# Optimization experiments

Hardware: AMD Instinct MI355X
Metric: run time of the kernel (lower is better)

Reference implementation:

```python
import jax, jax.numpy as jnp
import numpy as np

HIDDEN = 1024
NUM_HEAD = 16
HEAD_DIM = HIDDEN // NUM_HEAD


def setup_inputs() -> dict:
    key = jax.random.key(0)
    ks = jax.random.split(key, 9)
    B, S = 1, 4096
    scale = 1.0 / np.sqrt(HIDDEN)
    inp = {
        "x": jax.random.normal(ks[0], (B, S, HIDDEN), dtype=jnp.float32),
        "wq": jax.random.normal(ks[1], (HIDDEN, HIDDEN), dtype=jnp.float32) * scale,
        "bq": jnp.zeros((HIDDEN,), dtype=jnp.float32),
        "wk": jax.random.normal(ks[2], (HIDDEN, HIDDEN), dtype=jnp.float32) * scale,
        "bk": jnp.zeros((HIDDEN,), dtype=jnp.float32),
        "wv": jax.random.normal(ks[3], (HIDDEN, HIDDEN), dtype=jnp.float32) * scale,
        "bv": jnp.zeros((HIDDEN,), dtype=jnp.float32),
        "wo": jax.random.normal(ks[4], (HIDDEN, HIDDEN), dtype=jnp.float32) * scale,
        "bo": jnp.zeros((HIDDEN,), dtype=jnp.float32),
    }
    return inp


def reference(x, wq, bq, wk, bk, wv, bv, wo, bo):
    B, S, _ = x.shape
    # QKV projections (torch Linear: x @ W.T + b)
    def split_heads(t):
        return t.reshape(B, S, NUM_HEAD, HEAD_DIM).transpose(0, 2, 1, 3)  # [B,H,S,D]
    q = split_heads(x @ wq.T + bq)
    k = split_heads(x @ wk.T + bk)
    v = split_heads(x @ wv.T + bv)
    # scaled dot-product scores: [B,H,S,S]
    scores = jnp.einsum('bhsd,bhtd->bhst', q, k) / jnp.sqrt(jnp.float32(HEAD_DIM))
    # faithful double softmax over the key axis (no mask; dropout = eval identity)
    attn = jax.nn.softmax(scores, axis=-1)
    attn = jax.nn.softmax(attn, axis=-1)
    out = jnp.einsum('bhst,bhtd->bhsd', attn, v)  # [B,H,S,D]
    out = out.transpose(0, 2, 1, 3).reshape(B, S, HIDDEN)
    return out @ wo.T + bo
```

## Files before the change

### kernel.cpp

```cpp
#include <hip/hip_runtime.h>
#include <hip/hip_bf16.h>
#include <stdint.h>

#define S 4096
#define HID 1024
#define NH 16
#define DH 64

typedef __attribute__((ext_vector_type(8))) short short8;
typedef __attribute__((ext_vector_type(4))) float f32x4;
typedef __attribute__((ext_vector_type(16))) float f32x16;
typedef __attribute__((ext_vector_type(4))) unsigned int u32x4;

__device__ __forceinline__ unsigned short f2bf(float f) {
  unsigned int u = __builtin_bit_cast(unsigned int, f);
  u += 0x7FFF + ((u >> 16) & 1);
  return (unsigned short)(u >> 16);
}
__device__ __forceinline__ unsigned int pktrunc(float lo, float hi) {
  return __builtin_amdgcn_perm(__builtin_bit_cast(unsigned int, hi),
                               __builtin_bit_cast(unsigned int, lo), 0x07060302u);
}
__device__ __forceinline__ void gload16(const unsigned short* g, unsigned short* l) {
  __builtin_amdgcn_global_load_lds((const __attribute__((address_space(1))) unsigned int*)g,
                                   (__attribute__((address_space(3))) unsigned int*)l, 16, 0, 0);
}

__global__ __launch_bounds__(256) void cast_kernel(
    const float* __restrict__ x,  const float* __restrict__ wq,
    const float* __restrict__ wk, const float* __restrict__ wv,
    const float* __restrict__ wo,
    unsigned short* __restrict__ xb,  unsigned short* __restrict__ wqb,
    unsigned short* __restrict__ wkb, unsigned short* __restrict__ wvb,
    unsigned short* __restrict__ wob)
{
  int y = blockIdx.y;
  const float* src; unsigned short* dst; int n;
  if      (y == 0) { src = x;  dst = xb;  n = S * HID; }
  else if (y == 1) { src = wq; dst = wqb; n = HID * HID; }
  else if (y == 2) { src = wk; dst = wkb; n = HID * HID; }
  else if (y == 3) { src = wv; dst = wvb; n = HID * HID; }
  else             { src = wo; dst = wob; n = HID * HID; }
  int i = (blockIdx.x * 256 + threadIdx.x) * 4;
  if (i < n) {
    float4 v = *reinterpret_cast<const float4*>(src + i);
    ushort4 o;
    o.x = f2bf(v.x); o.y = f2bf(v.y); o.z = f2bf(v.z); o.w = f2bf(v.w);
    *reinterpret_cast<ushort4*>(dst + i) = o;
  }
}

__device__ __forceinline__ void gemm128(
    const unsigned short* __restrict__ A, const unsigned short* __restrict__ W,
    unsigned short* As, unsigned short* Bs, f32x4 acc[4][4], int row0, int col0)
{
  const int tid = threadIdx.x;
  const int wave = tid >> 6, lane = tid & 63, quad = lane >> 4, l16 = lane & 15;
  const int wr = (wave >> 1) * 64, wc = (wave & 1) * 64;
  const int srow = lane >> 2, sseg = lane & 3;
  const f32x4 z = {0.f, 0.f, 0.f, 0.f};
  #pragma unroll
  for (int i = 0; i < 4; i++)
    #pragma unroll
    for (int j = 0; j < 4; j++) acc[i][j] = z;

  for (int k0 = 0; k0 < HID; k0 += 32) {
    __syncthreads();
    #pragma unroll
    for (int c = 0; c < 2; c++) {
      const int rbase = c * 64 + wave * 16;
      gload16(A + (size_t)(row0 + rbase + srow) * HID + k0 + sseg * 8, As + rbase * 32);
      gload16(W + (size_t)(col0 + rbase + srow) * HID + k0 + sseg * 8, Bs + rbase * 32);
    }
    __syncthreads();

    short8 af[4], bfr[4];
    #pragma unroll
    for (int i = 0; i < 4; i++)
      af[i] = *reinterpret_cast<const short8*>(As + (wr + i * 16 + l16) * 32 + quad * 8);
    #pragma unroll
    for (int j = 0; j < 4; j++)
      bfr[j] = *reinterpret_cast<const short8*>(Bs + (wc + j * 16 + l16) * 32 + quad * 8);
    #pragma unroll
    for (int i = 0; i < 4; i++)
      #pragma unroll
      for (int j = 0; j < 4; j++)
        acc[i][j] = __builtin_amdgcn_mfma_f32_16x16x32_bf16(af[i], bfr[j], acc[i][j], 0, 0, 0);
  }
}

__global__ __launch_bounds__(256) void qkv_gemm_kernel(
    const unsigned short* __restrict__ X,
    const unsigned short* __restrict__ Wq, const unsigned short* __restrict__ Wk,
    const unsigned short* __restrict__ Wv,
    const float* __restrict__ bq, const float* __restrict__ bk, const float* __restrict__ bv,
    unsigned short* __restrict__ Qo, unsigned short* __restrict__ K2o, unsigned short* __restrict__ Vbo)
{
  __shared__ unsigned short As[128 * 32];
  __shared__ unsigned short Bs[128 * 32];
  const int zsel = blockIdx.z;
  const unsigned short* W = (zsel == 0) ? Wq : (zsel == 1) ? Wk : Wv;
  const float* bias        = (zsel == 0) ? bq : (zsel == 1) ? bk : bv;
  const int row0 = blockIdx.x * 128, col0 = blockIdx.y * 128;
  f32x4 acc[4][4];
  gemm128(X, W, As, Bs, acc, row0, col0);

  const int tid = threadIdx.x;
  const int wave = tid >> 6, lane = tid & 63, quad = lane >> 4, l16 = lane & 15;
  const int wr = (wave >> 1) * 64, wc = (wave & 1) * 64;

  if (zsel == 0) {
    const float osc = 0.18033688011112042f;
    #pragma unroll
    for (int j = 0; j < 4; j++) {
      int n = col0 + wc + j * 16 + l16;
      float bb = bias[n];
      int h = n >> 6, d = n & 63;
      #pragma unroll
      for (int i = 0; i < 4; i++)
        #pragma unroll
        for (int rr = 0; rr < 4; rr++) {
          int s = row0 + wr + i * 16 + quad * 4 + rr;
          Qo[(size_t)(h * S + s) * DH + d] = f2bf((acc[i][j][rr] + bb) * osc);
        }
    }
  } else if (zsel == 1) {
    #pragma unroll
    for (int j = 0; j < 4; j++) {
      int n = col0 + wc + j * 16 + l16;
      float bb = bias[n];
      int h = n >> 6, dh = n & 63;
      int c = dh >> 4, hfk = (dh >> 3) & 1, j8 = dh & 7;
      #pragma unroll
      for (int i = 0; i < 4; i++)
        #pragma unroll
        for (int rr = 0; rr < 4; rr++) {
          int s = row0 + wr + i * 16 + quad * 4 + rr;
          int g = s >> 5, l32k = s & 31;
          K2o[((size_t)((h * 128 + g) * 4 + c) * 64 + hfk * 32 + l32k) * 8 + j8] =
              f2bf(acc[i][j][rr] + bb);
        }
    }
  } else {
    #pragma unroll
    for (int j = 0; j < 4; j++) {
      int n = col0 + wc + j * 16 + l16;
      float bb = bias[n];
      int h = n >> 6, dh = n & 63;
      int ng = dh >> 5, l32v = dh & 31;
      int hf_v = quad & 1, jj0 = (quad >> 1) * 4;
      #pragma unroll
      for (int i = 0; i < 4; i++) {
        int gt = (row0 + wr + i * 16) >> 5;
        int grp = i & 1;
        ushort4 pv;
        pv.x = f2bf(acc[i][j][0] + bb); pv.y = f2bf(acc[i][j][1] + bb);
        pv.z = f2bf(acc[i][j][2] + bb); pv.w = f2bf(acc[i][j][3] + bb);
        *reinterpret_cast<ushort4*>(
            Vbo + ((size_t)(((h * 128 + gt) * 2 + grp) * 2 + ng) * 64 + hf_v * 32 + l32v) * 8 + jj0) = pv;
      }
    }
  }
}

__global__ __launch_bounds__(256) void out_gemm_kernel(
    const unsigned short* __restrict__ A, const unsigned short* __restrict__ W,
    const float* __restrict__ be, float* __restrict__ dst)
{
  __shared__ unsigned short As[128 * 32];
  __shared__ unsigned short Bs[128 * 32];
  const int row0 = blockIdx.x * 128, col0 = blockIdx.y * 128;
  f32x4 acc[4][4];
  gemm128(A, W, As, Bs, acc, row0, col0);

  const int tid = threadIdx.x;
  const int wave = tid >> 6, lane = tid & 63, quad = lane >> 4, l16 = lane & 15;
  const int wr = (wave >> 1) * 64, wc = (wave & 1) * 64;
  #pragma unroll
  for (int j = 0; j < 4; j++) {
    int n = col0 + wc + j * 16 + l16;
    float bb = be[n];
    #pragma unroll
    for (int i = 0; i < 4; i++)
      #pragma unroll
      for (int rr = 0; rr < 4; rr++) {
        int s = row0 + wr + i * 16 + quad * 4 + rr;
        dst[(size_t)s * HID + n] = acc[i][j][rr] + bb;
      }
  }
}

__global__ __launch_bounds__(256) void vsum_kernel(
    const unsigned short* __restrict__ Vb, float* __restrict__ VsumP)
{
  __shared__ float red[256];
  const int p = blockIdx.x, h = blockIdx.y, tid = threadIdx.x;
  const int d = tid & 63, chunk = tid >> 6;
  const int ng = d >> 5, l32 = d & 31;
  float s = 0.f;
  for (int m = 0; m < 4; m++) {
    int gt = p * 16 + chunk * 4 + m;
    #pragma unroll
    for (int grp = 0; grp < 2; grp++)
      #pragma unroll
      for (int hf = 0; hf < 2; hf++) {
        uint4 u = *reinterpret_cast<const uint4*>(
            Vb + ((size_t)(((h * 128 + gt) * 2 + grp) * 2 + ng) * 64 + hf * 32 + l32) * 8);
        const unsigned int w[4] = {u.x, u.y, u.z, u.w};
        #pragma unroll
        for (int q = 0; q < 4; q++) {
          s += __builtin_bit_cast(float, w[q] << 16);
          s += __builtin_bit_cast(float, w[q] & 0xFFFF0000u);
        }
      }
  }
  red[tid] = s;
  __syncthreads();
  if (tid < 64)
    VsumP[p * 1024 + h * 64 + tid] = red[tid] + red[64 + tid] + red[128 + tid] + red[192 + tid];
}

__global__ __launch_bounds__(256) void biasfold_kernel(
    const float* __restrict__ VsumP, const float* __restrict__ wo,
    const float* __restrict__ bo, float* __restrict__ be)
{
  const int n = blockIdx.x * 4 + (threadIdx.x >> 6);
  const int l = threadIdx.x & 63;
  float acc = 0.f;
  #pragma unroll
  for (int i = 0; i < 16; i++) {
    float vs = 0.f;
    #pragma unroll
    for (int p = 0; p < 8; p++) vs += VsumP[p * 1024 + l + 64 * i];
    acc += vs * wo[(size_t)n * HID + l + 64 * i];
  }
  #pragma unroll
  for (int off = 32; off >= 1; off >>= 1) acc += __shfl_xor(acc, off);
  if (l == 0) be[n] = bo[n] + acc * (1.f / 4097.f);
}

__global__ __launch_bounds__(256, 4) void attn_kernel(
    const unsigned short* __restrict__ Q, const unsigned short* __restrict__ K2,
    const unsigned short* __restrict__ Vb, unsigned short* __restrict__ OUT)
{
  __shared__ float Ol[2][32][64];
  __shared__ float Z1l[128];

  const int h = blockIdx.y, q0 = blockIdx.x * 64;
  const int tid = threadIdx.x;
  const int wave = tid >> 6, lane = tid & 63, hf = lane >> 5, l32 = lane & 31;
  const int qc = wave & 1, ks = wave >> 1;

  short8 qf[4];
  {
    const unsigned short* qrow = Q + (size_t)(h * S + q0 + qc * 32 + l32) * DH;
    #pragma unroll
    for (int c = 0; c < 4; c++)
      qf[c] = *reinterpret_cast<const short8*>(qrow + c * 16 + hf * 8);
  }

  float z1p = 0.f;
  f32x16 Oa[2];
  #pragma unroll
  for (int ng = 0; ng < 2; ng++)
    #pragma unroll
    for (int r = 0; r < 16; r++) Oa[ng][r] = 0.f;

  const unsigned short* Kb = K2 + (size_t)h * 128 * 4 * 64 * 8;
  const unsigned short* Vbb = Vb + (size_t)h * 128 * 4 * 64 * 8;

  const int g0 = ks * 64, g1 = g0 + 64;
  for (int g = g0; g < g1; g++) {
    short8 kf[4];
    #pragma unroll
    for (int c = 0; c < 4; c++)
      kf[c] = *reinterpret_cast<const short8*>(Kb + ((size_t)(g * 4 + c) * 64 + lane) * 8);
    short8 vfr[2][2];
    #pragma unroll
    for (int grp = 0; grp < 2; grp++)
      #pragma unroll
      for (int ng = 0; ng < 2; ng++)
        vfr[grp][ng] = *reinterpret_cast<const short8*>(
            Vbb + ((size_t)((g * 2 + grp) * 2 + ng) * 64 + lane) * 8);

    f32x16 acc;
    #pragma unroll
    for (int r = 0; r < 16; r++) acc[r] = 0.f;
    #pragma unroll
    for (int c = 0; c < 4; c++)
      acc = __builtin_amdgcn_mfma_f32_32x32x16_bf16(kf[c], qf[c], acc, 0, 0, 0);

    unsigned int D[8];
    #pragma unroll
    for (int m = 0; m < 8; m++) {
      float t0 = __builtin_amdgcn_exp2f(acc[2 * m]);
      float t1 = __builtin_amdgcn_exp2f(acc[2 * m + 1]);
      z1p += t0 + t1;
      D[m] = pktrunc(t0, t1);
    }
    u32x4 d0 = {D[0], D[1], D[2], D[3]};
    u32x4 d1 = {D[4], D[5], D[6], D[7]};
    short8 A0 = __builtin_bit_cast(short8, d0);
    short8 A1 = __builtin_bit_cast(short8, d1);

    Oa[0] = __builtin_amdgcn_mfma_f32_32x32x16_bf16(A0, vfr[0][0], Oa[0], 0, 0, 0);
    Oa[1] = __builtin_amdgcn_mfma_f32_32x32x16_bf16(A0, vfr[0][1], Oa[1], 0, 0, 0);
    Oa[0] = __builtin_amdgcn_mfma_f32_32x32x16_bf16(A1, vfr[1][0], Oa[0], 0, 0, 0);
    Oa[1] = __builtin_amdgcn_mfma_f32_32x32x16_bf16(A1, vfr[1][1], Oa[1], 0, 0, 0);
  }

  {
    float z1 = z1p + __shfl_xor(z1p, 32);
    if (hf == 0) Z1l[ks * 64 + qc * 32 + l32] = z1;
  }
  if (ks == 0) {
    #pragma unroll
    for (int reg = 0; reg < 16; reg++) {
      const int row = (reg & 3) + 8 * (reg >> 2) + 4 * hf;
      #pragma unroll
      for (int ng = 0; ng < 2; ng++)
        Ol[qc][row][ng * 32 + l32] = Oa[ng][reg];
    }
  }
  __syncthreads();
  if (ks == 1) {
    #pragma unroll
    for (int reg = 0; reg < 16; reg++) {
      const int row = (reg & 3) + 8 * (reg >> 2) + 4 * hf;
      const int ql = qc * 32 + row;
      const float rz = 1.f / ((Z1l[ql] + Z1l[64 + ql]) * 4097.f);
      const int s = q0 + ql;
      #pragma unroll
      for (int ng = 0; ng < 2; ng++) {
        const float o = Ol[qc][row][ng * 32 + l32] + Oa[ng][reg];
        OUT[(size_t)s * HID + h * DH + ng * 32 + l32] = f2bf(o * rz);
      }
    }
  }
}

extern "C" void kernel_launch(void* const* d_in, const int* in_sizes, int n_in,
                              void* d_out, int out_size, void* d_ws, size_t ws_size,
                              hipStream_t stream) {
  const float* x  = (const float*)d_in[0];
  const float* wq = (const float*)d_in[1];
  const float* bq = (const float*)d_in[2];
  const float* wk = (const float*)d_in[3];
  const float* bk = (const float*)d_in[4];
  const float* wv = (const float*)d_in[5];
  const float* bv = (const float*)d_in[6];
  const float* wo = (const float*)d_in[7];
  const float* bo = (const float*)d_in[8];
  float* out = (float*)d_out;

  char* ws = (char*)d_ws;
  unsigned short* xb  = (unsigned short*)(ws);
  unsigned short* wqb = (unsigned short*)(ws + (8u  << 20));
  unsigned short* wkb = (unsigned short*)(ws + (10u << 20));
  unsigned short* wvb = (unsigned short*)(ws + (12u << 20));
  unsigned short* wob = (unsigned short*)(ws + (14u << 20));
  unsigned short* qw  = (unsigned short*)(ws + (16u << 20));
  unsigned short* k2  = (unsigned short*)(ws + (24u << 20));
  unsigned short* vb  = (unsigned short*)(ws + (32u << 20));
  float* vsump        = (float*)(ws + (40u << 20));
  float* be           = (float*)(ws + (40u << 20) + 65536);
  unsigned short* aw  = xb;

  cast_kernel<<<dim3(4096, 5), 256, 0, stream>>>(x, wq, wk, wv, wo, xb, wqb, wkb, wvb, wob);
  qkv_gemm_kernel<<<dim3(32, 8, 3), 256, 0, stream>>>(xb, wqb, wkb, wvb, bq, bk, bv, qw, k2, vb);
  vsum_kernel<<<dim3(8, 16), 256, 0, stream>>>(vb, vsump);
  biasfold_kernel<<<dim3(256), 256, 0, stream>>>(vsump, wo, bo, be);
  attn_kernel<<<dim3(64, 16), 256, 0, stream>>>(qw, k2, vb, aw);
  out_gemm_kernel<<<dim3(32, 8, 1), 256, 0, stream>>>(aw, wob, be, out);
}
```

Before: 253.4 us.

## Swap GEMM operands for vectorized epilogues, split attention keys four ways, grid-stride cast

```diff
diff --git a/kernel.cpp b/kernel.cpp
--- a/kernel.cpp
+++ b/kernel.cpp
@@ -16,6 +16,10 @@
   unsigned int u = __builtin_bit_cast(unsigned int, f);
   u += 0x7FFF + ((u >> 16) & 1);
   return (unsigned short)(u >> 16);
+}
+__device__ __forceinline__ float bf2f(unsigned short b) {
+  unsigned int u = ((unsigned int)b) << 16;
+  return __builtin_bit_cast(float, u);
 }
 __device__ __forceinline__ unsigned int pktrunc(float lo, float hi) {
   return __builtin_amdgcn_perm(__builtin_bit_cast(unsigned int, hi),
@@ -41,8 +45,8 @@
   else if (y == 2) { src = wk; dst = wkb; n = HID * HID; }
   else if (y == 3) { src = wv; dst = wvb; n = HID * HID; }
   else             { src = wo; dst = wob; n = HID * HID; }
-  int i = (blockIdx.x * 256 + threadIdx.x) * 4;
-  if (i < n) {
+  const int stride = 1024 * 256 * 4;
+  for (int i = (blockIdx.x * 256 + threadIdx.x) * 4; i < n; i += stride) {
     float4 v = *reinterpret_cast<const float4*>(src + i);
     ushort4 o;
     o.x = f2bf(v.x); o.y = f2bf(v.y); o.z = f2bf(v.z); o.w = f2bf(v.w);
@@ -99,49 +103,60 @@
   __shared__ unsigned short As[128 * 32];
   __shared__ unsigned short Bs[128 * 32];
   const int zsel = blockIdx.z;
-  const unsigned short* W = (zsel == 0) ? Wq : (zsel == 1) ? Wk : Wv;
-  const float* bias        = (zsel == 0) ? bq : (zsel == 1) ? bk : bv;
-  const int row0 = blockIdx.x * 128, col0 = blockIdx.y * 128;
-  f32x4 acc[4][4];
-  gemm128(X, W, As, Bs, acc, row0, col0);
+  const unsigned short* Wmat = (zsel == 0) ? Wq : (zsel == 1) ? Wk : Wv;
+  const float* bias           = (zsel == 0) ? bq : (zsel == 1) ? bk : bv;
 
   const int tid = threadIdx.x;
   const int wave = tid >> 6, lane = tid & 63, quad = lane >> 4, l16 = lane & 15;
   const int wr = (wave >> 1) * 64, wc = (wave & 1) * 64;
 
-  if (zsel == 0) {
-    const float osc = 0.18033688011112042f;
-    #pragma unroll
-    for (int j = 0; j < 4; j++) {
-      int n = col0 + wc + j * 16 + l16;
-      float bb = bias[n];
-      int h = n >> 6, d = n & 63;
-      #pragma unroll
-      for (int i = 0; i < 4; i++)
+  f32x4 acc[4][4];
+  if (zsel < 2) {
+    const int row0 = blockIdx.y * 128, col0 = blockIdx.x * 128;
+    gemm128(Wmat, X, As, Bs, acc, row0, col0);
+
+    if (zsel == 0) {
+      const float osc = 0.18033688011112042f;
+      #pragma unroll
+      for (int i = 0; i < 4; i++) {
+        const int n0 = row0 + wr + i * 16 + quad * 4;
+        const float4 b4 = *reinterpret_cast<const float4*>(bias + n0);
+        const int h = n0 >> 6, d0 = n0 & 63;
         #pragma unroll
-        for (int rr = 0; rr < 4; rr++) {
-          int s = row0 + wr + i * 16 + quad * 4 + rr;
-          Qo[(size_t)(h * S + s) * DH + d] = f2bf((acc[i][j][rr] + bb) * osc);
+        for (int j = 0; j < 4; j++) {
+          const int s = col0 + wc + j * 16 + l16;
+          ushort4 o;
+          o.x = f2bf((acc[i][j][0] + b4.x) * osc);
+          o.y = f2bf((acc[i][j][1] + b4.y) * osc);
+          o.z = f2bf((acc[i][j][2] + b4.z) * osc);
+          o.w = f2bf((acc[i][j][3] + b4.w) * osc);
+          *reinterpret_cast<ushort4*>(Qo + (size_t)(h * S + s) * DH + d0) = o;
         }
-    }
-  } else if (zsel == 1) {
-    #pragma unroll
-    for (int j = 0; j < 4; j++) {
-      int n = col0 + wc + j * 16 + l16;
-      float bb = bias[n];
-      int h = n >> 6, dh = n & 63;
-      int c = dh >> 4, hfk = (dh >> 3) & 1, j8 = dh & 7;
-      #pragma unroll
-      for (int i = 0; i < 4; i++)
+      }
+    } else {
+      #pragma unroll
+      for (int i = 0; i < 4; i++) {
+        const int n0 = row0 + wr + i * 16 + quad * 4;
+        const float4 b4 = *reinterpret_cast<const float4*>(bias + n0);
+        const int h = n0 >> 6, dh0 = n0 & 63;
+        const int c = dh0 >> 4, hfk = (dh0 >> 3) & 1, j80 = dh0 & 7;
         #pragma unroll
-        for (int rr = 0; rr < 4; rr++) {
-          int s = row0 + wr + i * 16 + quad * 4 + rr;
-          int g = s >> 5, l32k = s & 31;
-          K2o[((size_t)((h * 128 + g) * 4 + c) * 64 + hfk * 32 + l32k) * 8 + j8] =
-              f2bf(acc[i][j][rr] + bb);
+        for (int j = 0; j < 4; j++) {
+          const int s = col0 + wc + j * 16 + l16;
+          const int g = s >> 5, l32k = s & 31;
+          ushort4 o;
+          o.x = f2bf(acc[i][j][0] + b4.x);
+          o.y = f2bf(acc[i][j][1] + b4.y);
+          o.z = f2bf(acc[i][j][2] + b4.z);
+          o.w = f2bf(acc[i][j][3] + b4.w);
+          *reinterpret_cast<ushort4*>(
+              K2o + ((size_t)((h * 128 + g) * 4 + c) * 64 + hfk * 32 + l32k) * 8 + j80) = o;
         }
+      }
     }
   } else {
+    const int row0 = blockIdx.x * 128, col0 = blockIdx.y * 128;
+    gemm128(X, Wmat, As, Bs, acc, row0, col0);
     #pragma unroll
     for (int j = 0; j < 4; j++) {
       int n = col0 + wc + j * 16 + l16;
@@ -164,29 +179,30 @@
 }
 
 __global__ __launch_bounds__(256) void out_gemm_kernel(
-    const unsigned short* __restrict__ A, const unsigned short* __restrict__ W,
+    const unsigned short* __restrict__ Aattn, const unsigned short* __restrict__ Wo,
     const float* __restrict__ be, float* __restrict__ dst)
 {
   __shared__ unsigned short As[128 * 32];
   __shared__ unsigned short Bs[128 * 32];
   const int row0 = blockIdx.x * 128, col0 = blockIdx.y * 128;
   f32x4 acc[4][4];
-  gemm128(A, W, As, Bs, acc, row0, col0);
+  gemm128(Wo, Aattn, As, Bs, acc, row0, col0);
 
   const int tid = threadIdx.x;
   const int wave = tid >> 6, lane = tid & 63, quad = lane >> 4, l16 = lane & 15;
   const int wr = (wave >> 1) * 64, wc = (wave & 1) * 64;
   #pragma unroll
-  for (int j = 0; j < 4; j++) {
-    int n = col0 + wc + j * 16 + l16;
-    float bb = be[n];
-    #pragma unroll
-    for (int i = 0; i < 4; i++)
-      #pragma unroll
-      for (int rr = 0; rr < 4; rr++) {
-        int s = row0 + wr + i * 16 + quad * 4 + rr;
-        dst[(size_t)s * HID + n] = acc[i][j][rr] + bb;
-      }
+  for (int i = 0; i < 4; i++) {
+    const int n0 = row0 + wr + i * 16 + quad * 4;
+    const float4 b4 = *reinterpret_cast<const float4*>(be + n0);
+    #pragma unroll
+    for (int j = 0; j < 4; j++) {
+      const int s = col0 + wc + j * 16 + l16;
+      float4 o;
+      o.x = acc[i][j][0] + b4.x; o.y = acc[i][j][1] + b4.y;
+      o.z = acc[i][j][2] + b4.z; o.w = acc[i][j][3] + b4.w;
+      *reinterpret_cast<float4*>(dst + (size_t)s * HID + n0) = o;
+    }
   }
 }
 
@@ -239,21 +255,20 @@
   if (l == 0) be[n] = bo[n] + acc * (1.f / 4097.f);
 }
 
-__global__ __launch_bounds__(256, 4) void attn_kernel(
+__global__ __launch_bounds__(256, 6) void attn_kernel(
     const unsigned short* __restrict__ Q, const unsigned short* __restrict__ K2,
     const unsigned short* __restrict__ Vb, unsigned short* __restrict__ OUT)
 {
-  __shared__ float Ol[2][32][64];
-  __shared__ float Z1l[128];
-
-  const int h = blockIdx.y, q0 = blockIdx.x * 64;
+  __shared__ unsigned short Olb[3][32][64];
+  __shared__ float Z1l[4][32];
+
+  const int h = blockIdx.y, q0 = blockIdx.x * 32;
   const int tid = threadIdx.x;
-  const int wave = tid >> 6, lane = tid & 63, hf = lane >> 5, l32 = lane & 31;
-  const int qc = wave & 1, ks = wave >> 1;
+  const int ks = tid >> 6, lane = tid & 63, hf = lane >> 5, l32 = lane & 31;
 
   short8 qf[4];
   {
-    const unsigned short* qrow = Q + (size_t)(h * S + q0 + qc * 32 + l32) * DH;
+    const unsigned short* qrow = Q + (size_t)(h * S + q0 + l32) * DH;
     #pragma unroll
     for (int c = 0; c < 4; c++)
       qf[c] = *reinterpret_cast<const short8*>(qrow + c * 16 + hf * 8);
@@ -266,10 +281,10 @@
     #pragma unroll
     for (int r = 0; r < 16; r++) Oa[ng][r] = 0.f;
 
-  const unsigned short* Kb = K2 + (size_t)h * 128 * 4 * 64 * 8;
+  const unsigned short* Kb  = K2 + (size_t)h * 128 * 4 * 64 * 8;
   const unsigned short* Vbb = Vb + (size_t)h * 128 * 4 * 64 * 8;
 
-  const int g0 = ks * 64, g1 = g0 + 64;
+  const int g0 = ks * 32, g1 = g0 + 32;
   for (int g = g0; g < g1; g++) {
     short8 kf[4];
     #pragma unroll
@@ -311,29 +326,31 @@
 
   {
     float z1 = z1p + __shfl_xor(z1p, 32);
-    if (hf == 0) Z1l[ks * 64 + qc * 32 + l32] = z1;
-  }
-  if (ks == 0) {
+    if (hf == 0) Z1l[ks][l32] = z1;
+  }
+  if (ks > 0) {
     #pragma unroll
     for (int reg = 0; reg < 16; reg++) {
       const int row = (reg & 3) + 8 * (reg >> 2) + 4 * hf;
       #pragma unroll
       for (int ng = 0; ng < 2; ng++)
-        Ol[qc][row][ng * 32 + l32] = Oa[ng][reg];
+        Olb[ks - 1][row][ng * 32 + l32] = f2bf(Oa[ng][reg]);
     }
   }
   __syncthreads();
-  if (ks == 1) {
+  if (ks == 0) {
     #pragma unroll
     for (int reg = 0; reg < 16; reg++) {
       const int row = (reg & 3) + 8 * (reg >> 2) + 4 * hf;
-      const int ql = qc * 32 + row;
-      const float rz = 1.f / ((Z1l[ql] + Z1l[64 + ql]) * 4097.f);
-      const int s = q0 + ql;
+      const float zt = Z1l[0][row] + Z1l[1][row] + Z1l[2][row] + Z1l[3][row];
+      const float rz = 1.f / (zt * 4097.f);
+      const int s = q0 + row;
       #pragma unroll
       for (int ng = 0; ng < 2; ng++) {
-        const float o = Ol[qc][row][ng * 32 + l32] + Oa[ng][reg];
-        OUT[(size_t)s * HID + h * DH + ng * 32 + l32] = f2bf(o * rz);
+        const int d = ng * 32 + l32;
+        const float o = Oa[ng][reg] + bf2f(Olb[0][row][d]) + bf2f(Olb[1][row][d])
+                                    + bf2f(Olb[2][row][d]);
+        OUT[(size_t)s * HID + h * DH + d] = f2bf(o * rz);
       }
     }
   }
@@ -366,10 +383,10 @@
   float* be           = (float*)(ws + (40u << 20) + 65536);
   unsigned short* aw  = xb;
 
-  cast_kernel<<<dim3(4096, 5), 256, 0, stream>>>(x, wq, wk, wv, wo, xb, wqb, wkb, wvb, wob);
+  cast_kernel<<<dim3(1024, 5), 256, 0, stream>>>(x, wq, wk, wv, wo, xb, wqb, wkb, wvb, wob);
   qkv_gemm_kernel<<<dim3(32, 8, 3), 256, 0, stream>>>(xb, wqb, wkb, wvb, bq, bk, bv, qw, k2, vb);
   vsum_kernel<<<dim3(8, 16), 256, 0, stream>>>(vb, vsump);
   biasfold_kernel<<<dim3(256), 256, 0, stream>>>(vsump, wo, bo, be);
-  attn_kernel<<<dim3(64, 16), 256, 0, stream>>>(qw, k2, vb, aw);
-  out_gemm_kernel<<<dim3(32, 8, 1), 256, 0, stream>>>(aw, wob, be, out);
-}
+  attn_kernel<<<dim3(128, 16), 256, 0, stream>>>(qw, k2, vb, aw);
+  out_gemm_kernel<<<dim3(8, 32), 256, 0, stream>>>(aw, wob, be, out);
+}
```

Measured after the change: 308.1 us. 21.6% more time.
